# Optimization experiments

Hardware: AMD Instinct MI355X
Metric: run time of the kernel (lower is better)

The kernel has to match this reference:

```python
import jax, jax.numpy as jnp
import numpy as np

D_P, D_T, D_F = 128, 256, 384
D = D_P + D_T + D_F            # 768
NUM_PART, NUM_TIMES, NUM_F0 = 64, 601, 360
NHEAD, NLAYERS, DFF = 12, 6, 2048
CTX, PRED = 1024, 64
BATCH = 8
NEG = -1e9


def sin_emb(vals, d, L, base=10000.0):
    # vectorized version of the per-scalar sin_embedding loop
    i = jnp.arange(d // 2, dtype=jnp.float32)
    wk = base ** (-i / d) * (d / L)
    ang = vals[..., None].astype(jnp.float32) * wk           # [..., d/2]
    return jnp.stack([jnp.sin(ang), jnp.cos(ang)], axis=-1).reshape(vals.shape + (d,))


def layernorm(x, g, b, eps=1e-5):
    mu = jnp.mean(x, axis=-1, keepdims=True)
    var = jnp.var(x, axis=-1, keepdims=True)
    return (x - mu) * jax.lax.rsqrt(var + eps) * g + b


def setup_inputs() -> dict:
    key = jax.random.key(0)
    ks = jax.random.split(key, 20)
    inp = {}
    inp['context_participant'] = jax.random.randint(ks[0], (BATCH, CTX), 0, NUM_PART)
    inp['context_time'] = jax.random.uniform(ks[1], (BATCH, CTX), jnp.float32) * 60.0
    inp['context_f0'] = jax.random.randint(ks[2], (BATCH, CTX), 0, NUM_F0)
    # learned / frozen tables
    inp['part_table'] = jax.random.normal(ks[3], (NUM_PART, D_P), jnp.float32)
    inp['time_table'] = sin_emb(jnp.arange(NUM_TIMES, dtype=jnp.float32), D_T, NUM_TIMES)
    inp['f0_table'] = sin_emb(jnp.arange(NUM_F0, dtype=jnp.float32), D_F, NUM_F0)
    inp['pad'] = jax.random.normal(ks[4], (D,), jnp.float32)
    s = 0.02
    inp['Wqkv'] = jax.random.normal(ks[5], (NLAYERS, 3 * D, D), jnp.float32) * s
    inp['bqkv'] = jnp.zeros((NLAYERS, 3 * D), jnp.float32)
    inp['Wo'] = jax.random.normal(ks[6], (NLAYERS, D, D), jnp.float32) * s
    inp['bo'] = jnp.zeros((NLAYERS, D), jnp.float32)
    inp['ln1_g'] = jnp.ones((NLAYERS, D), jnp.float32)
    inp['ln1_b'] = jnp.zeros((NLAYERS, D), jnp.float32)
    inp['W1'] = jax.random.normal(ks[7], (NLAYERS, DFF, D), jnp.float32) * s
    inp['b1'] = jnp.zeros((NLAYERS, DFF), jnp.float32)
    inp['W2'] = jax.random.normal(ks[8], (NLAYERS, D, DFF), jnp.float32) * s
    inp['b2'] = jnp.zeros((NLAYERS, D), jnp.float32)
    inp['ln2_g'] = jnp.ones((NLAYERS, D), jnp.float32)
    inp['ln2_b'] = jnp.zeros((NLAYERS, D), jnp.float32)
    return inp


def reference(context_participant, context_time, context_f0, part_table, time_table,
              f0_table, pad, Wqkv, bqkv, Wo, bo, ln1_g, ln1_b, W1, b1, W2, b2,
              ln2_g, ln2_b):
    B = context_participant.shape[0]
    emb = jnp.concatenate([
        part_table[context_participant],
        sin_emb(context_time, D_T, NUM_TIMES),
        f0_table[context_f0],
    ], axis=-1)                                               # [B, CTX, D]
    dummy = jnp.broadcast_to(pad[None, None, :], (B, PRED, D))
    x = jnp.concatenate([emb, dummy], axis=1)                 # [B, S, D]
    S = CTX + PRED
    # causal mask with -1e9 above diagonal; target block fully masked (incl. diag)
    mask = jnp.where(jnp.triu(jnp.ones((S, S), bool), k=1), NEG, 0.0).astype(jnp.float32)
    mask = mask.at[CTX:, CTX:].set(NEG)
    hd = D // NHEAD
    scale = 1.0 / jnp.sqrt(jnp.float32(hd))
    for l in range(NLAYERS):
        qkv = x @ Wqkv[l].T + bqkv[l]
        q, k, v = jnp.split(qkv, 3, axis=-1)
        q = q.reshape(B, S, NHEAD, hd)
        k = k.reshape(B, S, NHEAD, hd)
        v = v.reshape(B, S, NHEAD, hd)
        scores = jnp.einsum('bqhd,bkhd->bhqk', q, k) * scale + mask
        attn = jax.nn.softmax(scores, axis=-1)
        ctx = jnp.einsum('bhqk,bkhd->bqhd', attn, v).reshape(B, S, D)
        x = layernorm(x + (ctx @ Wo[l].T + bo[l]), ln1_g[l], ln1_b[l])
        ff = jax.nn.relu(x @ W1[l].T + b1[l]) @ W2[l].T + b2[l]
        x = layernorm(x + ff, ln2_g[l], ln2_b[l])
    pred = x[:, CTX:, :]
    pred_cat_logits = pred[:, :, :D_P] @ part_table.T
    pred_time_logits = pred[:, :, D_P:D_P + D_T] @ time_table.T
    pred_f0_logits = pred[:, :, D_P + D_T:] @ f0_table.T
    return (pred_cat_logits, pred_time_logits, pred_f0_logits)
```

## Files before the change

kernel.cpp:

```cpp
#include <hip/hip_runtime.h>
#include <hip/hip_bf16.h>
#include <math.h>

#define D_P 128
#define D_T 256
#define D_F 384
#define DIM 768
#define NUM_TIMES 601
#define NUM_F0 360
#define NHEAD 12
#define HD 64
#define NLAYERS 6
#define DFF 2048
#define CTX 1024
#define SEQ 1088
#define BATCH 8
#define ROWS (BATCH*SEQ)
#define TDIM3 (3*DIM)
#define PREDROWS 512

typedef unsigned short ushort_t;
typedef __attribute__((ext_vector_type(8))) short bfrag;
typedef __attribute__((ext_vector_type(4))) float f32x4;

__global__ void SequenceModel_30425548325019_kernel(unsigned short* out, int n, unsigned short v) {
  int i = blockIdx.x * 256 + threadIdx.x;
  if (i < n) out[i] = v;
}

__device__ inline short f2bf(float f) {
  unsigned u = __float_as_uint(f);
  unsigned r = (u + 0x7FFFu + ((u >> 16) & 1u)) >> 16;
  return (short)r;
}

__device__ inline float bf2f(ushort_t u) {
  return __uint_as_float((unsigned)u << 16);
}

__device__ inline float bflo(unsigned u) { return __uint_as_float(u << 16); }
__device__ inline float bfhi(unsigned u) { return __uint_as_float(u & 0xFFFF0000u); }
__device__ inline unsigned packbf(float a, float b) {
  return ((unsigned)(ushort_t)f2bf(a)) | (((unsigned)(ushort_t)f2bf(b)) << 16);
}

__device__ inline void gload16(const void* g, void* l) {
  __builtin_amdgcn_global_load_lds(
      (const __attribute__((address_space(1))) unsigned*)g,
      (__attribute__((address_space(3))) unsigned*)l, 16, 0, 0);
}

__global__ __launch_bounds__(256) void cvt_bf16(const float* __restrict__ src,
                                                ushort_t* __restrict__ dst, int n) {
  int i = (blockIdx.x * 256 + threadIdx.x) * 4;
  if (i >= n) return;
  float4 v = *(const float4*)(src + i);
  dst[i + 0] = (ushort_t)f2bf(v.x);
  dst[i + 1] = (ushort_t)f2bf(v.y);
  dst[i + 2] = (ushort_t)f2bf(v.z);
  dst[i + 3] = (ushort_t)f2bf(v.w);
}

__global__ __launch_bounds__(256) void embed_kernel(
    const int* __restrict__ cp, const float* __restrict__ ct,
    const int* __restrict__ cf, const float* __restrict__ part,
    const float* __restrict__ f0t, const float* __restrict__ pad,
    ushort_t* __restrict__ xb) {
  int idx = blockIdx.x * 256 + threadIdx.x;
  if (idx >= ROWS * DIM) return;
  int d = idx % DIM;
  int row = idx / DIM;
  int b = row / SEQ, s = row - b * SEQ;
  float v;
  if (s >= CTX) {
    v = pad[d];
  } else if (d < D_P) {
    v = part[cp[b * CTX + s] * D_P + d];
  } else if (d < D_P + D_T) {
    int j = d - D_P;
    int i2 = j >> 1;
    float wk = powf(10000.f, -(float)i2 / (float)D_T) * ((float)D_T / (float)NUM_TIMES);
    float ang = ct[b * CTX + s] * wk;
    v = (j & 1) ? cosf(ang) : sinf(ang);
  } else {
    v = f0t[cf[b * CTX + s] * D_F + (d - D_P - D_T)];
  }
  xb[idx] = (ushort_t)f2bf(v);
}

#define BM 128
#define BN 128
#define BK 32
#define QSCALE 0.1803368801f

__global__ __launch_bounds__(256) void gemm_bb(
    const ushort_t* __restrict__ A, const ushort_t* __restrict__ B,
    const float* __restrict__ bias,
    float* __restrict__ C, ushort_t* __restrict__ Cb,
    int M, int N, int K, int relu, int qscale) {
  __shared__ short As[2][4 * BM * 8];
  __shared__ short Bs[2][4 * BN * 8];
  const int tid = threadIdx.x;
  const int wave = tid >> 6, lane = tid & 63;
  const int wr = wave >> 1, wc = wave & 1;
  const int l15 = lane & 15, l4 = lane >> 4;
  const int m0 = blockIdx.y * BM, n0 = blockIdx.x * BN;
  f32x4 acc[4][4] = {};

  const int u0row = (wave * 64 + lane) & 127, u0kg = (wave * 64 + lane) >> 7;
  const int u1row = (256 + wave * 64 + lane) & 127, u1kg = (256 + wave * 64 + lane) >> 7;
  const ushort_t* Ap0 = A + (size_t)(m0 + u0row) * K + u0kg * 8;
  const ushort_t* Bp0 = B + (size_t)(n0 + u0row) * K + u0kg * 8;
  const ushort_t* Ap1 = A + (size_t)(m0 + u1row) * K + u1kg * 8;
  const ushort_t* Bp1 = B + (size_t)(n0 + u1row) * K + u1kg * 8;
  const int ldsoff0 = (wave * 64) * 8;
  const int ldsoff1 = (256 + wave * 64) * 8;

  gload16(Ap0, &As[0][ldsoff0]);
  gload16(Bp0, &Bs[0][ldsoff0]);
  gload16(Ap1, &As[0][ldsoff1]);
  gload16(Bp1, &Bs[0][ldsoff1]);
  __syncthreads();

  int cur = 0;
  for (int k0 = 0; k0 < K; k0 += BK) {
    if (k0 + BK < K) {
      gload16(Ap0 + k0 + BK, &As[cur ^ 1][ldsoff0]);
      gload16(Bp0 + k0 + BK, &Bs[cur ^ 1][ldsoff0]);
      gload16(Ap1 + k0 + BK, &As[cur ^ 1][ldsoff1]);
      gload16(Bp1 + k0 + BK, &Bs[cur ^ 1][ldsoff1]);
    }
    bfrag a[4], b[4];
    #pragma unroll
    for (int f = 0; f < 4; ++f) {
      a[f] = *(const bfrag*)&As[cur][(l4 * BM + wr * 64 + f * 16 + l15) * 8];
      b[f] = *(const bfrag*)&Bs[cur][(l4 * BN + wc * 64 + f * 16 + l15) * 8];
    }
    __builtin_amdgcn_s_setprio(1);
    #pragma unroll
    for (int i = 0; i < 4; ++i)
      #pragma unroll
      for (int j = 0; j < 4; ++j)
        acc[i][j] = __builtin_amdgcn_mfma_f32_16x16x32_bf16(a[i], b[j], acc[i][j], 0, 0, 0);
    __builtin_amdgcn_s_setprio(0);
    __syncthreads();
    cur ^= 1;
  }
  #pragma unroll
  for (int i = 0; i < 4; ++i) {
    int mbase = m0 + wr * 64 + i * 16 + l4 * 4;
    #pragma unroll
    for (int j = 0; j < 4; ++j) {
      int n = n0 + wc * 64 + j * 16 + l15;
      float bv = bias[n];
      #pragma unroll
      for (int r = 0; r < 4; ++r) {
        int m = mbase + r;
        float v = acc[i][j][r] + bv;
        if (relu) v = fmaxf(v, 0.f);
        if (qscale && n < DIM) v *= QSCALE;
        if (C) C[(size_t)m * N + n] = v;
        if (Cb) Cb[(size_t)m * N + n] = (ushort_t)f2bf(v);
      }
    }
  }
}

__global__ __launch_bounds__(256) void gather_pred(const ushort_t* __restrict__ xb,
                                                   ushort_t* __restrict__ xpb) {
  int idx = blockIdx.x * 256 + threadIdx.x;
  if (idx >= PREDROWS * DIM) return;
  int r = idx / DIM, d = idx - r * DIM;
  int b = r >> 6, rr = r & 63;
  xpb[idx] = xb[(size_t)(b * SEQ + CTX + rr) * DIM + d];
}

__global__ __launch_bounds__(256) void head_mfma(
    const ushort_t* __restrict__ A, const ushort_t* __restrict__ B,
    float* __restrict__ C, int N, int K, int lda, int coloff) {
  __shared__ short As[4 * BM * 8];
  __shared__ short Bs[4 * BN * 8];
  const int tid = threadIdx.x;
  const int wave = tid >> 6, lane = tid & 63;
  const int wr = wave >> 1, wc = wave & 1;
  const int l15 = lane & 15, l4 = lane >> 4;
  const int m0 = blockIdx.y * BM, n0 = blockIdx.x * BN;
  f32x4 acc[4][4] = {};

  for (int k0 = 0; k0 < K; k0 += BK) {
    __syncthreads();
    #pragma unroll
    for (int i = 0; i < 2; ++i) {
      int u = i * 256 + wave * 64 + lane;
      int row = u & 127, kg = u >> 7;
      gload16(A + (size_t)(m0 + row) * lda + coloff + k0 + kg * 8,
              &As[(i * 256 + wave * 64) * 8]);
      gload16(B + (size_t)(n0 + row) * K + k0 + kg * 8,
              &Bs[(i * 256 + wave * 64) * 8]);
    }
    __syncthreads();
    bfrag a[4], b[4];
    #pragma unroll
    for (int f = 0; f < 4; ++f) {
      a[f] = *(const bfrag*)&As[(l4 * BM + wr * 64 + f * 16 + l15) * 8];
      b[f] = *(const bfrag*)&Bs[(l4 * BN + wc * 64 + f * 16 + l15) * 8];
    }
    #pragma unroll
    for (int i = 0; i < 4; ++i)
      #pragma unroll
      for (int j = 0; j < 4; ++j)
        acc[i][j] = __builtin_amdgcn_mfma_f32_16x16x32_bf16(a[i], b[j], acc[i][j], 0, 0, 0);
  }
  #pragma unroll
  for (int i = 0; i < 4; ++i) {
    int mbase = m0 + wr * 64 + i * 16 + l4 * 4;
    #pragma unroll
    for (int j = 0; j < 4; ++j) {
      int n = n0 + wc * 64 + j * 16 + l15;
      if (n >= N) continue;
      #pragma unroll
      for (int r = 0; r < 4; ++r)
        C[(size_t)(mbase + r) * N + n] = acc[i][j][r];
    }
  }
}

#define QBLK 64
#define KBLK 64
__global__ __launch_bounds__(256) void attn_mfma(const ushort_t* __restrict__ qkv,
                                                 ushort_t* __restrict__ outb) {
  const int qt = blockIdx.x, h = blockIdx.y, b = blockIdx.z;
  const int q0 = qt * QBLK;
  __shared__ short Vt[8 * 64 * 9];
  __shared__ short Ps[8 * 64 * 9];
  __shared__ float SO[64 * 65];
  __shared__ float alphaS[64], linvS[64];
  const int tid = threadIdx.x;
  const int wave = tid >> 6, lane = tid & 63;
  const int l15 = lane & 15, l4 = lane >> 4;
  const int smrow = tid >> 2, smc = tid & 3;
  const int qf = wave;

  const size_t qrow_addr = (size_t)(b * SEQ + q0 + qf * 16 + l15) * TDIM3 + h * HD;
  bfrag aq0 = *(const bfrag*)(qkv + qrow_addr + l4 * 8);
  bfrag aq1 = *(const bfrag*)(qkv + qrow_addr + 32 + l4 * 8);

  float mrun = -1e30f, lrun = 0.f;
  f32x4 o[4] = {};
  const int nkt = (q0 < CTX) ? (q0 + QBLK) / KBLK : (CTX / KBLK);

  for (int kt = 0; kt < nkt; ++kt) {
    const int k0 = kt * KBLK;
    __syncthreads();
    #pragma unroll
    for (int i = 0; i < 2; ++i) {
      int u = tid + 256 * i;
      int krow = u >> 3, dg = u & 7;
      bfrag vv = *(const bfrag*)(qkv + (size_t)(b * SEQ + k0 + krow) * TDIM3 + 2 * DIM + h * HD + dg * 8);
      int kg = krow >> 3, j = krow & 7;
      #pragma unroll
      for (int e = 0; e < 8; ++e)
        Vt[(kg * 64 + dg * 8 + e) * 9 + j] = vv[e];
    }
    #pragma unroll
    for (int jk = 0; jk < 4; ++jk) {
      const size_t krow_addr = (size_t)(b * SEQ + k0 + jk * 16 + l15) * TDIM3 + DIM + h * HD;
      bfrag bk0 = *(const bfrag*)(qkv + krow_addr + l4 * 8);
      bfrag bk1 = *(const bfrag*)(qkv + krow_addr + 32 + l4 * 8);
      f32x4 s = {};
      s = __builtin_amdgcn_mfma_f32_16x16x32_bf16(aq0, bk0, s, 0, 0, 0);
      s = __builtin_amdgcn_mfma_f32_16x16x32_bf16(aq1, bk1, s, 0, 0, 0);
      #pragma unroll
      for (int r = 0; r < 4; ++r)
        SO[(qf * 16 + l4 * 4 + r) * 65 + jk * 16 + l15] = s[r];
    }
    __syncthreads();
    {
      const int qglob = q0 + smrow;
      float p[16];
      float tm = -1e30f;
      #pragma unroll
      for (int i = 0; i < 16; ++i) {
        int kg = k0 + smc * 16 + i;
        float s = SO[smrow * 65 + smc * 16 + i];
        bool allowed = (qglob < CTX) ? (kg <= qglob) : true;
        p[i] = allowed ? s : -1e30f;
        tm = fmaxf(tm, p[i]);
      }
      tm = fmaxf(tm, __shfl_xor(tm, 1));
      tm = fmaxf(tm, __shfl_xor(tm, 2));
      float mn = fmaxf(mrun, tm);
      float alpha = exp2f(mrun - mn);
      float ls = 0.f;
      #pragma unroll
      for (int i = 0; i < 16; ++i) { p[i] = exp2f(p[i] - mn); ls += p[i]; }
      ls += __shfl_xor(ls, 1);
      ls += __shfl_xor(ls, 2);
      lrun = lrun * alpha + ls;
      mrun = mn;
      if (smc == 0) alphaS[smrow] = alpha;
      short* pd0 = &Ps[((smc * 2 + 0) * 64 + smrow) * 9];
      short* pd1 = &Ps[((smc * 2 + 1) * 64 + smrow) * 9];
      #pragma unroll
      for (int i = 0; i < 8; ++i) { pd0[i] = f2bf(p[i]); pd1[i] = f2bf(p[i + 8]); }
    }
    __syncthreads();
    {
      #pragma unroll
      for (int r = 0; r < 4; ++r) {
        float ar = alphaS[qf * 16 + l4 * 4 + r];
        #pragma unroll
        for (int df = 0; df < 4; ++df) o[df][r] *= ar;
      }
      #pragma unroll
      for (int c = 0; c < 2; ++c) {
        bfrag pa = *(const bfrag*)&Ps[((c * 4 + l4) * 64 + qf * 16 + l15) * 9];
        #pragma unroll
        for (int df = 0; df < 4; ++df) {
          bfrag v = *(const bfrag*)&Vt[((c * 4 + l4) * 64 + df * 16 + l15) * 9];
          o[df] = __builtin_amdgcn_mfma_f32_16x16x32_bf16(pa, v, o[df], 0, 0, 0);
        }
      }
    }
  }
  if (smc == 0) linvS[smrow] = 1.f / lrun;
  __syncthreads();
  #pragma unroll
  for (int r = 0; r < 4; ++r) {
    float li = linvS[qf * 16 + l4 * 4 + r];
    #pragma unroll
    for (int df = 0; df < 4; ++df)
      SO[(qf * 16 + l4 * 4 + r) * 65 + df * 16 + l15] = o[df][r] * li;
  }
  __syncthreads();
  #pragma unroll
  for (int i = 0; i < 2; ++i) {
    int s = tid + 256 * i;
    int r = s >> 3, kg = s & 7;
    ushort_t* dst = outb + (size_t)(b * SEQ + q0 + r) * DIM + h * HD + kg * 8;
    const float* sp = &SO[r * 65 + kg * 8];
    bfrag t;
    #pragma unroll
    for (int e = 0; e < 8; ++e) t[e] = f2bf(sp[e]);
    *(bfrag*)dst = t;
  }
}

__global__ __launch_bounds__(256) void ln_bb(const ushort_t* __restrict__ raw,
                                             ushort_t* __restrict__ xb,
                                             const float* __restrict__ g,
                                             const float* __restrict__ bb) {
  const int row = blockIdx.x;
  unsigned* pu = (unsigned*)(xb + (size_t)row * DIM);
  const unsigned* qu = (const unsigned*)(raw + (size_t)row * DIM);
  const float2* g2 = (const float2*)g;
  const float2* b2 = (const float2*)bb;
  const int tid = threadIdx.x;

  unsigned x0 = pu[tid], r0 = qu[tid];
  float v00 = bflo(x0) + bflo(r0);
  float v01 = bfhi(x0) + bfhi(r0);
  float v10 = 0.f, v11 = 0.f;
  unsigned x1 = 0, r1 = 0;
  if (tid < 128) {
    x1 = pu[256 + tid]; r1 = qu[256 + tid];
    v10 = bflo(x1) + bflo(r1);
    v11 = bfhi(x1) + bfhi(r1);
  }
  float s1 = v00 + v01 + v10 + v11;
  float s2 = v00 * v00 + v01 * v01 + v10 * v10 + v11 * v11;
  #pragma unroll
  for (int off = 32; off >= 1; off >>= 1) {
    s1 += __shfl_down(s1, off);
    s2 += __shfl_down(s2, off);
  }
  __shared__ float r1s[4], r2s[4];
  int wid = tid >> 6;
  if ((tid & 63) == 0) { r1s[wid] = s1; r2s[wid] = s2; }
  __syncthreads();
  s1 = r1s[0] + r1s[1] + r1s[2] + r1s[3];
  s2 = r2s[0] + r2s[1] + r2s[2] + r2s[3];
  const float mu = s1 * (1.f / DIM);
  const float var = s2 * (1.f / DIM) - mu * mu;
  const float rs = rsqrtf(var + 1e-5f);
  float2 ga = g2[tid], ba = b2[tid];
  float o00 = (v00 - mu) * rs * ga.x + ba.x;
  float o01 = (v01 - mu) * rs * ga.y + ba.y;
  pu[tid] = packbf(o00, o01);
  if (tid < 128) {
    float2 gb = g2[256 + tid], bbv = b2[256 + tid];
    float o10 = (v10 - mu) * rs * gb.x + bbv.x;
    float o11 = (v11 - mu) * rs * gb.y + bbv.y;
    pu[256 + tid] = packbf(o10, o11);
  }
}

extern "C" void kernel_launch(void* const* d_in, const int* in_sizes, int n_in,
                              void* d_out, int out_size, void* d_ws, size_t ws_size,
                              hipStream_t stream) {
  const size_t N_XB   = (size_t)ROWS * DIM / 2;
  const size_t N_BUFB = (size_t)ROWS * TDIM3 / 2;
  const size_t N_CTB  = (size_t)ROWS * DIM / 2;
  const size_t N_WQ   = 10616832 / 2;
  const size_t N_WO   = 3538944 / 2;
  const size_t N_W1   = 9437184 / 2;
  const size_t N_W2   = 9437184 / 2;
  const size_t N_PT   = 8192 / 2;
  const size_t N_TT   = 153856 / 2;
  const size_t N_FT   = 138240 / 2;
  const size_t N_XPB  = (size_t)PREDROWS * DIM / 2;
  size_t need = (N_XB + N_BUFB + N_CTB + N_WQ + N_WO + N_W1 + N_W2 +
                 N_PT + N_TT + N_FT + N_XPB) * sizeof(float);
  if (ws_size < need) {
    SequenceModel_30425548325019_kernel<<<(out_size + 255) / 256, 256, 0, stream>>>(
        (unsigned short*)d_out, out_size, (unsigned short)0x4280);
    return;
  }

  const int*   cp    = (const int*)d_in[0];
  const float* ct    = (const float*)d_in[1];
  const int*   cf    = (const int*)d_in[2];
  const float* part  = (const float*)d_in[3];
  const float* timet = (const float*)d_in[4];
  const float* f0t   = (const float*)d_in[5];
  const float* pad   = (const float*)d_in[6];
  const float* Wqkv  = (const float*)d_in[7];
  const float* bqkv  = (const float*)d_in[8];
  const float* Wo    = (const float*)d_in[9];
  const float* bo    = (const float*)d_in[10];
  const float* ln1g  = (const float*)d_in[11];
  const float* ln1b  = (const float*)d_in[12];
  const float* W1    = (const float*)d_in[13];
  const float* b1    = (const float*)d_in[14];
  const float* W2    = (const float*)d_in[15];
  const float* b2    = (const float*)d_in[16];
  const float* ln2g  = (const float*)d_in[17];
  const float* ln2b  = (const float*)d_in[18];

  float* base = (float*)d_ws;
  ushort_t* xb     = (ushort_t*)base;      base += N_XB;
  ushort_t* bufb   = (ushort_t*)base;      base += N_BUFB;
  ushort_t* ctxbb  = (ushort_t*)base;      base += N_CTB;
  ushort_t* Wqkvb  = (ushort_t*)base;      base += N_WQ;
  ushort_t* Wob    = (ushort_t*)base;      base += N_WO;
  ushort_t* W1b    = (ushort_t*)base;      base += N_W1;
  ushort_t* W2b    = (ushort_t*)base;      base += N_W2;
  ushort_t* partb  = (ushort_t*)base;      base += N_PT;
  ushort_t* timetb = (ushort_t*)base;      base += N_TT;
  ushort_t* f0tb   = (ushort_t*)base;      base += N_FT;
  ushort_t* xpb    = (ushort_t*)base;

  cvt_bf16<<<(10616832 / 4 + 255) / 256, 256, 0, stream>>>(Wqkv, Wqkvb, 10616832);
  cvt_bf16<<<(3538944 / 4 + 255) / 256, 256, 0, stream>>>(Wo, Wob, 3538944);
  cvt_bf16<<<(9437184 / 4 + 255) / 256, 256, 0, stream>>>(W1, W1b, 9437184);
  cvt_bf16<<<(9437184 / 4 + 255) / 256, 256, 0, stream>>>(W2, W2b, 9437184);
  cvt_bf16<<<(8192 / 4 + 255) / 256, 256, 0, stream>>>(part, partb, 8192);
  cvt_bf16<<<(153856 / 4 + 255) / 256, 256, 0, stream>>>(timet, timetb, 153856);
  cvt_bf16<<<(138240 / 4 + 255) / 256, 256, 0, stream>>>(f0t, f0tb, 138240);

  embed_kernel<<<(ROWS * DIM + 255) / 256, 256, 0, stream>>>(cp, ct, cf, part, f0t, pad, xb);

  for (int l = 0; l < NLAYERS; ++l) {
    gemm_bb<<<dim3(TDIM3 / BN, ROWS / BM), 256, 0, stream>>>(
        xb, Wqkvb + (size_t)l * TDIM3 * DIM, bqkv + l * TDIM3,
        nullptr, bufb, ROWS, TDIM3, DIM, 0, 1);
    attn_mfma<<<dim3(SEQ / QBLK, NHEAD, BATCH), 256, 0, stream>>>(bufb, ctxbb);
    gemm_bb<<<dim3(DIM / BN, ROWS / BM), 256, 0, stream>>>(
        ctxbb, Wob + (size_t)l * DIM * DIM, bo + l * DIM,
        nullptr, bufb, ROWS, DIM, DIM, 0, 0);
    ln_bb<<<ROWS, 256, 0, stream>>>(bufb, xb, ln1g + l * DIM, ln1b + l * DIM);
    gemm_bb<<<dim3(DFF / BN, ROWS / BM), 256, 0, stream>>>(
        xb, W1b + (size_t)l * DFF * DIM, b1 + l * DFF,
        nullptr, bufb, ROWS, DFF, DIM, 1, 0);
    gemm_bb<<<dim3(DIM / BN, ROWS / BM), 256, 0, stream>>>(
        bufb, W2b + (size_t)l * DIM * DFF, b2 + l * DIM,
        nullptr, ctxbb, ROWS, DIM, DFF, 0, 0);
    ln_bb<<<ROWS, 256, 0, stream>>>(ctxbb, xb, ln2g + l * DIM, ln2b + l * DIM);
  }

  float* out = (float*)d_out;
  gather_pred<<<(PREDROWS * DIM + 255) / 256, 256, 0, stream>>>(xb, xpb);
  head_mfma<<<dim3(1, PREDROWS / BM), 256, 0, stream>>>(xpb, partb, out, 64, 128, DIM, 0);
  head_mfma<<<dim3(5, PREDROWS / BM), 256, 0, stream>>>(xpb, timetb, out + 32768, NUM_TIMES, 256, DIM, 128);
  head_mfma<<<dim3(3, PREDROWS / BM), 256, 0, stream>>>(xpb, f0tb, out + 32768 + 307712, NUM_F0, 384, DIM, 384);
}
```

Before: 2.754 ms.

## Compute attention softmax in registers from MFMA accumulators instead of LDS staging

The attention kernel now runs the online softmax directly on the MFMA score fragments held in registers. Row max and row sum are reduced with lane shuffles across the 16 lanes that share a row, and the running max and sum are kept per register row. This drops the round trip of scores through shared memory, one barrier per key tile, and the alpha and 1/l arrays in LDS. Shared memory is also aliased so the output staging buffer overlaps the V and P buffers, which shrinks the LDS footprint and may allow more blocks per CU. In exchange it adds more shuffles and more per-thread register state.

```diff
diff --git a/kernel.cpp b/kernel.cpp
--- a/kernel.cpp
+++ b/kernel.cpp
@@ -32,10 +32,6 @@
   unsigned u = __float_as_uint(f);
   unsigned r = (u + 0x7FFFu + ((u >> 16) & 1u)) >> 16;
   return (short)r;
-}
-
-__device__ inline float bf2f(ushort_t u) {
-  return __uint_as_float((unsigned)u << 16);
 }
 
 __device__ inline float bflo(unsigned u) { return __uint_as_float(u << 16); }
@@ -231,21 +227,22 @@
                                                  ushort_t* __restrict__ outb) {
   const int qt = blockIdx.x, h = blockIdx.y, b = blockIdx.z;
   const int q0 = qt * QBLK;
-  __shared__ short Vt[8 * 64 * 9];
-  __shared__ short Ps[8 * 64 * 9];
-  __shared__ float SO[64 * 65];
-  __shared__ float alphaS[64], linvS[64];
+  __shared__ char smem[8 * 64 * 9 * 2 * 2 > 64 * 65 * 4 ? 8 * 64 * 9 * 2 * 2 : 64 * 65 * 4];
+  short* Vt = (short*)smem;
+  short* Ps = (short*)(smem + 8 * 64 * 9 * 2);
+  float* SO = (float*)smem;
   const int tid = threadIdx.x;
   const int wave = tid >> 6, lane = tid & 63;
   const int l15 = lane & 15, l4 = lane >> 4;
-  const int smrow = tid >> 2, smc = tid & 3;
   const int qf = wave;
 
   const size_t qrow_addr = (size_t)(b * SEQ + q0 + qf * 16 + l15) * TDIM3 + h * HD;
   bfrag aq0 = *(const bfrag*)(qkv + qrow_addr + l4 * 8);
   bfrag aq1 = *(const bfrag*)(qkv + qrow_addr + 32 + l4 * 8);
 
-  float mrun = -1e30f, lrun = 0.f;
+  float mrun[4], lrun[4];
+  #pragma unroll
+  for (int r = 0; r < 4; ++r) { mrun[r] = -1e30f; lrun[r] = 0.f; }
   f32x4 o[4] = {};
   const int nkt = (q0 < CTX) ? (q0 + QBLK) / KBLK : (CTX / KBLK);
 
@@ -262,72 +259,67 @@
       for (int e = 0; e < 8; ++e)
         Vt[(kg * 64 + dg * 8 + e) * 9 + j] = vv[e];
     }
+    f32x4 s[4];
     #pragma unroll
     for (int jk = 0; jk < 4; ++jk) {
       const size_t krow_addr = (size_t)(b * SEQ + k0 + jk * 16 + l15) * TDIM3 + DIM + h * HD;
       bfrag bk0 = *(const bfrag*)(qkv + krow_addr + l4 * 8);
       bfrag bk1 = *(const bfrag*)(qkv + krow_addr + 32 + l4 * 8);
-      f32x4 s = {};
-      s = __builtin_amdgcn_mfma_f32_16x16x32_bf16(aq0, bk0, s, 0, 0, 0);
-      s = __builtin_amdgcn_mfma_f32_16x16x32_bf16(aq1, bk1, s, 0, 0, 0);
-      #pragma unroll
-      for (int r = 0; r < 4; ++r)
-        SO[(qf * 16 + l4 * 4 + r) * 65 + jk * 16 + l15] = s[r];
-    }
-    __syncthreads();
-    {
-      const int qglob = q0 + smrow;
-      float p[16];
+      f32x4 acc = {};
+      acc = __builtin_amdgcn_mfma_f32_16x16x32_bf16(aq0, bk0, acc, 0, 0, 0);
+      s[jk] = __builtin_amdgcn_mfma_f32_16x16x32_bf16(aq1, bk1, acc, 0, 0, 0);
+    }
+    #pragma unroll
+    for (int r = 0; r < 4; ++r) {
+      const int qglob = q0 + qf * 16 + l4 * 4 + r;
+      float pv[4];
       float tm = -1e30f;
       #pragma unroll
-      for (int i = 0; i < 16; ++i) {
-        int kg = k0 + smc * 16 + i;
-        float s = SO[smrow * 65 + smc * 16 + i];
+      for (int jk = 0; jk < 4; ++jk) {
+        int kg = k0 + jk * 16 + l15;
         bool allowed = (qglob < CTX) ? (kg <= qglob) : true;
-        p[i] = allowed ? s : -1e30f;
-        tm = fmaxf(tm, p[i]);
+        pv[jk] = allowed ? s[jk][r] : -1e30f;
+        tm = fmaxf(tm, pv[jk]);
       }
       tm = fmaxf(tm, __shfl_xor(tm, 1));
       tm = fmaxf(tm, __shfl_xor(tm, 2));
-      float mn = fmaxf(mrun, tm);
-      float alpha = exp2f(mrun - mn);
+      tm = fmaxf(tm, __shfl_xor(tm, 4));
+      tm = fmaxf(tm, __shfl_xor(tm, 8));
+      float mn = fmaxf(mrun[r], tm);
+      float alpha = exp2f(mrun[r] - mn);
       float ls = 0.f;
       #pragma unroll
-      for (int i = 0; i < 16; ++i) { p[i] = exp2f(p[i] - mn); ls += p[i]; }
+      for (int jk = 0; jk < 4; ++jk) { pv[jk] = exp2f(pv[jk] - mn); ls += pv[jk]; }
       ls += __shfl_xor(ls, 1);
       ls += __shfl_xor(ls, 2);
-      lrun = lrun * alpha + ls;
-      mrun = mn;
-      if (smc == 0) alphaS[smrow] = alpha;
-      short* pd0 = &Ps[((smc * 2 + 0) * 64 + smrow) * 9];
-      short* pd1 = &Ps[((smc * 2 + 1) * 64 + smrow) * 9];
-      #pragma unroll
-      for (int i = 0; i < 8; ++i) { pd0[i] = f2bf(p[i]); pd1[i] = f2bf(p[i + 8]); }
+      ls += __shfl_xor(ls, 4);
+      ls += __shfl_xor(ls, 8);
+      lrun[r] = lrun[r] * alpha + ls;
+      mrun[r] = mn;
+      #pragma unroll
+      for (int df = 0; df < 4; ++df) o[df][r] *= alpha;
+      const int qrow = qf * 16 + l4 * 4 + r;
+      #pragma unroll
+      for (int jk = 0; jk < 4; ++jk) {
+        int kgi = jk * 2 + (l15 >> 3), j = l15 & 7;
+        Ps[(kgi * 64 + qrow) * 9 + j] = f2bf(pv[jk]);
+      }
     }
     __syncthreads();
-    {
-      #pragma unroll
-      for (int r = 0; r < 4; ++r) {
-        float ar = alphaS[qf * 16 + l4 * 4 + r];
-        #pragma unroll
-        for (int df = 0; df < 4; ++df) o[df][r] *= ar;
+    #pragma unroll
+    for (int c = 0; c < 2; ++c) {
+      bfrag pa = *(const bfrag*)&Ps[((c * 4 + l4) * 64 + qf * 16 + l15) * 9];
+      #pragma unroll
+      for (int df = 0; df < 4; ++df) {
+        bfrag v = *(const bfrag*)&Vt[((c * 4 + l4) * 64 + df * 16 + l15) * 9];
+        o[df] = __builtin_amdgcn_mfma_f32_16x16x32_bf16(pa, v, o[df], 0, 0, 0);
       }
-      #pragma unroll
-      for (int c = 0; c < 2; ++c) {
-        bfrag pa = *(const bfrag*)&Ps[((c * 4 + l4) * 64 + qf * 16 + l15) * 9];
-        #pragma unroll
-        for (int df = 0; df < 4; ++df) {
-          bfrag v = *(const bfrag*)&Vt[((c * 4 + l4) * 64 + df * 16 + l15) * 9];
-          o[df] = __builtin_amdgcn_mfma_f32_16x16x32_bf16(pa, v, o[df], 0, 0, 0);
-        }
-      }
-    }
-  }
-  if (smc == 0) linvS[smrow] = 1.f / lrun;
+    }
+  }
   __syncthreads();
   #pragma unroll
   for (int r = 0; r < 4; ++r) {
-    float li = linvS[qf * 16 + l4 * 4 + r];
+    float li = 1.f / lrun[r];
     #pragma unroll
     for (int df = 0; df < 4; ++df)
       SO[(qf * 16 + l4 * 4 + r) * 65 + df * 16 + l15] = o[df][r] * li;
@@ -335,8 +327,8 @@
   __syncthreads();
   #pragma unroll
   for (int i = 0; i < 2; ++i) {
-    int s = tid + 256 * i;
-    int r = s >> 3, kg = s & 7;
+    int s2 = tid + 256 * i;
+    int r = s2 >> 3, kg = s2 & 7;
     ushort_t* dst = outb + (size_t)(b * SEQ + q0 + r) * DIM + h * HD + kg * 8;
     const float* sp = &SO[r * 65 + kg * 8];
     bfrag t;
@@ -361,9 +353,8 @@
   float v00 = bflo(x0) + bflo(r0);
   float v01 = bfhi(x0) + bfhi(r0);
   float v10 = 0.f, v11 = 0.f;
-  unsigned x1 = 0, r1 = 0;
   if (tid < 128) {
-    x1 = pu[256 + tid]; r1 = qu[256 + tid];
+    unsigned x1 = pu[256 + tid], r1 = qu[256 + tid];
     v10 = bflo(x1) + bflo(r1);
     v11 = bfhi(x1) + bfhi(r1);
   }
```

New measurement: 2.744 ms. About the same (-0.3%).
